# Kernel tuning notes

Hardware: AMD Instinct MI355X
Metric: run time of the kernel (lower is better)

Reference implementation:

```python
import jax, jax.numpy as jnp
import numpy as np

NEG_SLOPE = 0.2
N_NODES = 51200      # batch 256 graphs x 200 nodes
NODE_PER_G = 200
IN_DIM = 200
HID = 64
HEADS = 4
N_CLASSES = 2
E_RAND = 16 * N_NODES


def setup_inputs() -> dict:
    key = jax.random.key(0)
    ks = jax.random.split(key, 12)
    feat = jax.random.normal(ks[0], (N_NODES, IN_DIM), dtype=jnp.float32)
    # random edges kept within each 200-node graph block + self-loops (no zero in-degree)
    g_off = (jnp.arange(E_RAND) % (N_NODES // NODE_PER_G)) * NODE_PER_G
    src = jax.random.randint(ks[1], (E_RAND,), 0, NODE_PER_G) + g_off
    dst = jax.random.randint(ks[2], (E_RAND,), 0, NODE_PER_G) + g_off
    loop = jnp.arange(N_NODES)
    src = jnp.concatenate([src, loop]).astype(jnp.int32)
    dst = jnp.concatenate([dst, loop]).astype(jnp.int32)
    s = 0.05
    W0 = jax.random.normal(ks[3], (IN_DIM, HEADS * HID), dtype=jnp.float32) * s
    al0 = jax.random.normal(ks[4], (HEADS, HID), dtype=jnp.float32) * s
    ar0 = jax.random.normal(ks[5], (HEADS, HID), dtype=jnp.float32) * s
    W1 = jax.random.normal(ks[6], (HEADS * HID, HEADS * HID), dtype=jnp.float32) * s
    al1 = jax.random.normal(ks[7], (HEADS, HID), dtype=jnp.float32) * s
    ar1 = jax.random.normal(ks[8], (HEADS, HID), dtype=jnp.float32) * s
    Wc = jax.random.normal(ks[9], (NODE_PER_G * HID, N_CLASSES), dtype=jnp.float32) * s
    bc = jnp.zeros((N_CLASSES,), dtype=jnp.float32)
    return {"feat": feat, "src": src, "dst": dst, "W0": W0, "al0": al0, "ar0": ar0,
            "W1": W1, "al1": al1, "ar1": ar1, "Wc": Wc, "bc": bc, "batch_size": 256}


def gat_conv(h, src, dst, W, al, ar, residual):
    N = h.shape[0]
    ft = (h @ W).reshape(N, HEADS, HID)                      # [N,H,D]
    el = jnp.einsum('nhd,hd->nh', ft, al)                    # [N,H]
    er = jnp.einsum('nhd,hd->nh', ft, ar)
    e = jax.nn.leaky_relu(el[src] + er[dst], NEG_SLOPE)      # [E,H]
    emax = jax.ops.segment_max(e, dst, num_segments=N)
    a = jnp.exp(e - emax[dst])
    denom = jax.ops.segment_sum(a, dst, num_segments=N)
    alpha = a / denom[dst]                                   # [E,H]
    out = jax.ops.segment_sum(alpha[:, :, None] * ft[src], dst, num_segments=N)
    if residual:
        out = out + h.reshape(N, HEADS, HID)                 # identity residual (in==H*D)
    return jax.nn.elu(out)                                   # [N,H,D]


def reference(feat, src, dst, W0, al0, ar0, W1, al1, ar1, Wc, bc, batch_size):
    h = gat_conv(feat, src, dst, W0, al0, ar0, residual=False)
    h = h.reshape(h.shape[0], HEADS * HID)                   # flatten(1)
    h = gat_conv(h, src, dst, W1, al1, ar1, residual=True)
    h = h.mean(axis=1)                                       # mean over heads -> [N,D]
    h = h.reshape(batch_size, -1)                            # [B, node*D]
    return h @ Wc + bc
```

## Files before the change

### kernel.cpp

```cpp
#include <hip/hip_runtime.h>
#include <hip/hip_bf16.h>
#include <hip/hip_fp16.h>

#define N_NODES_C   51200
#define NODE_PER_G  200
#define NGRAPH      256
#define HEADS       4
#define HID         64
#define FDIM        256
#define IN_DIM_C    200
#define E_RAND_C    819200
#define RAND_PER_G  3200
#define AWS         3208
#define NEG_SLOPE   0.2f

typedef _Float16 f16x8 __attribute__((ext_vector_type(8)));
typedef float    f32x4 __attribute__((ext_vector_type(4)));

__device__ __forceinline__ float leaky(float x) { return fmaxf(x, NEG_SLOPE * x); }

__global__ __launch_bounds__(256) void transpose_both(
    const float* __restrict__ W0, const float* __restrict__ W1,
    _Float16* __restrict__ W0t, _Float16* __restrict__ W1t)
{
    int k = blockIdx.x, n = threadIdx.x;
    if (k < IN_DIM_C)
        W0t[(size_t)n * IN_DIM_C + k] = (_Float16)W0[(size_t)k * FDIM + n];
    else {
        int kk = k - IN_DIM_C;
        W1t[(size_t)n * FDIM + kk] = (_Float16)W1[(size_t)kk * FDIM + n];
    }
}

__global__ __launch_bounds__(1024) void build_csr(
    const int* __restrict__ src, const int* __restrict__ dst,
    uchar2* __restrict__ egs, int* __restrict__ goff)
{
    __shared__ uchar2 s_e[RAND_PER_G];
    __shared__ int s_cnt[256];
    __shared__ int s_off[256];

    const int g = blockIdx.x, tid = threadIdx.x;
    const int node0 = g * NODE_PER_G;
    uchar2* egsp = egs + (size_t)g * RAND_PER_G;

    if (tid < 256) s_cnt[tid] = 0;
    __syncthreads();
    for (int e = tid; e < RAND_PER_G; e += 1024) {
        int eid = g + (e << 8);
        uchar2 ed = make_uchar2((unsigned char)(src[eid] - node0),
                                (unsigned char)(dst[eid] - node0));
        s_e[e] = ed;
        atomicAdd(&s_cnt[ed.y], 1);
    }
    __syncthreads();
    if (tid < 64) {
        const int base = tid << 2;
        int c0_ = s_cnt[base], c1 = s_cnt[base + 1];
        int c2 = s_cnt[base + 2], c3 = s_cnt[base + 3];
        s_cnt[base] = 0; s_cnt[base + 1] = 0;
        s_cnt[base + 2] = 0; s_cnt[base + 3] = 0;
        int s1 = c0_ + c1, s2 = s1 + c2, s3 = s2 + c3;
        int pre = s3;
#pragma unroll
        for (int d = 1; d < 64; d <<= 1) {
            int t = __shfl_up(pre, d);
            if (tid >= d) pre += t;
        }
        int excl = pre - s3;
        s_off[base]     = excl;
        s_off[base + 1] = excl + c0_;
        s_off[base + 2] = excl + s1;
        s_off[base + 3] = excl + s2;
    }
    __syncthreads();
    for (int e = tid; e < RAND_PER_G; e += 1024) {
        uchar2 ed = s_e[e];
        int pos = s_off[ed.y] + atomicAdd(&s_cnt[ed.y], 1);
        egsp[pos] = ed;
    }
    if (tid <= NODE_PER_G)
        goff[(size_t)g * 201 + tid] = s_off[tid];
}

__device__ __forceinline__ int swzoff(int m, int kg) {
    int pair = m >> 1;
    int slot = (((m & 1) << 2) | kg) ^ (pair & 7);
    return pair * 64 + slot * 8;
}

__device__ __forceinline__ f16x8 cvt8(float4 a, float4 b) {
    f16x8 r;
    r[0] = (_Float16)a.x; r[1] = (_Float16)a.y;
    r[2] = (_Float16)a.z; r[3] = (_Float16)a.w;
    r[4] = (_Float16)b.x; r[5] = (_Float16)b.y;
    r[6] = (_Float16)b.z; r[7] = (_Float16)b.w;
    return r;
}

template <bool L1>
__global__ __launch_bounds__(1024) void fused_gat(
    const void* __restrict__ A_, const _Float16* __restrict__ Bt, int K,
    const uchar2* __restrict__ egs, const int* __restrict__ goff,
    const float* __restrict__ al, const float* __restrict__ ar,
    const _Float16* __restrict__ hprev, const float* __restrict__ Wc,
    const float* __restrict__ bc, void* __restrict__ out_)
{
    __shared__ __align__(16) _Float16 s_ft[NODE_PER_G * FDIM];
    __shared__ __align__(16) unsigned s_aw[HEADS * AWS];
    __shared__ float s_el[NODE_PER_G * HEADS];
    __shared__ float s_er[NODE_PER_G * HEADS];
    __shared__ int   s_off[NODE_PER_G + 1];
    __shared__ float s_red[2];

    const int g = blockIdx.x, tid = threadIdx.x;
    const int node0 = g * NODE_PER_G;
    const int wave = tid >> 6, lane = tid & 63;
    const uchar2* egp = egs + (size_t)g * RAND_PER_G;

    if (tid < 2) s_red[tid] = 0.f;
    if (tid <= NODE_PER_G) s_off[tid] = goff[(size_t)g * 201 + tid];

    {
        _Float16* sA = (_Float16*)s_aw;
        _Float16* sB = (_Float16*)s_aw + 208 * 32;
        const int arow = tid >> 2;
        const int agk  = tid & 3;
        const int KC = (K + 31) >> 5;
        const int aoffL = swzoff(lane & 15, lane >> 4);
        const uint4 z4 = make_uint4(0u, 0u, 0u, 0u);

        f32x4 acc[4][4];
#pragma unroll
        for (int t = 0; t < 4; ++t)
#pragma unroll
            for (int ni = 0; ni < 4; ++ni) acc[t][ni] = (f32x4){0.f, 0.f, 0.f, 0.f};

        for (int kc = 0; kc < KC; ++kc) {
            const int k8 = kc * 32 + agk * 8;
            __syncthreads();
            if (arow < 208) {
                if constexpr (L1) {
                    const _Float16* A = (const _Float16*)A_;
                    uint4 v = (arow < NODE_PER_G && k8 + 8 <= K)
                        ? *(const uint4*)&A[(size_t)(node0 + arow) * K + k8] : z4;
                    *(uint4*)&sA[swzoff(arow, agk)] = v;
                } else {
                    const float* A = (const float*)A_;
                    float4 x = make_float4(0.f, 0.f, 0.f, 0.f), y = x;
                    if (arow < NODE_PER_G && k8 + 8 <= K) {
                        const float* pa = &A[(size_t)(node0 + arow) * K + k8];
                        x = *(const float4*)pa;
                        y = *(const float4*)(pa + 4);
                    }
                    *(f16x8*)&sA[swzoff(arow, agk)] = cvt8(x, y);
                }
            }
            {
                uint4 v = (k8 + 8 <= K)
                    ? *(const uint4*)&Bt[(size_t)arow * K + k8] : z4;
                *(uint4*)&sB[swzoff(arow, agk)] = v;
            }
            __syncthreads();
#pragma unroll
            for (int t = 0; t < 4; ++t) {
                const int task = wave * 4 + t;
                if (task < 52) {
                    const int m16 = task >> 2, n64 = task & 3;
                    f16x8 af = *(const f16x8*)&sA[aoffL + m16 * 512];
#pragma unroll
                    for (int ni = 0; ni < 4; ++ni) {
                        f16x8 bf = *(const f16x8*)&sB[aoffL + n64 * 2048 + ni * 512];
                        acc[t][ni] = __builtin_amdgcn_mfma_f32_16x16x32_f16(
                            af, bf, acc[t][ni], 0, 0, 0);
                    }
                }
            }
        }
        __syncthreads();
#pragma unroll
        for (int t = 0; t < 4; ++t) {
            const int task = wave * 4 + t;
            if (task < 52) {
                const int m16 = task >> 2, n64 = task & 3;
                const int r0 = m16 * 16 + ((lane >> 4) << 2);
                const int cc = n64 * 64 + (lane & 15);
#pragma unroll
                for (int ni = 0; ni < 4; ++ni)
#pragma unroll
                    for (int r = 0; r < 4; ++r) {
                        int row = r0 + r;
                        if (row < NODE_PER_G)
                            s_ft[row * FDIM + cc + ni * 16] =
                                (_Float16)acc[t][ni][r];
                    }
            }
        }
    }
    __syncthreads();

    {
        const int lh = lane >> 4, ld = (lane & 15) * 4;
        float4 alv = *(const float4*)&al[lh * HID + ld];
        float4 arv = *(const float4*)&ar[lh * HID + ld];
        for (int n = wave; n < NODE_PER_G; n += 16) {
            uint2 gr = *(const uint2*)&s_ft[n * FDIM + lane * 4];
            float2 f01 = __half22float2(*(__half2*)&gr.x);
            float2 f23 = __half22float2(*(__half2*)&gr.y);
            float pl = f01.x * alv.x + f01.y * alv.y + f23.x * alv.z + f23.y * alv.w;
            float pr = f01.x * arv.x + f01.y * arv.y + f23.x * arv.z + f23.y * arv.w;
#pragma unroll
            for (int m = 1; m < 16; m <<= 1) {
                pl += __shfl_xor(pl, m);
                pr += __shfl_xor(pr, m);
            }
            if ((lane & 15) == 0) {
                s_el[n * 4 + lh] = pl;
                s_er[n * 4 + lh] = pr;
            }
        }
    }
    __syncthreads();

    for (int e = tid; e < RAND_PER_G; e += 1024) {
        uchar2 ed = egp[e];
        float4 elv = *(const float4*)&s_el[ed.x * 4];
        float4 erv = *(const float4*)&s_er[ed.y * 4];
        unsigned sb = (unsigned)ed.x << 16;
        __half h0 = __float2half_rn(__expf(leaky(elv.x + erv.x)));
        __half h1 = __float2half_rn(__expf(leaky(elv.y + erv.y)));
        __half h2 = __float2half_rn(__expf(leaky(elv.z + erv.z)));
        __half h3 = __float2half_rn(__expf(leaky(elv.w + erv.w)));
        s_aw[e]           = sb | (unsigned)__half_as_ushort(h0);
        s_aw[AWS + e]     = sb | (unsigned)__half_as_ushort(h1);
        s_aw[2 * AWS + e] = sb | (unsigned)__half_as_ushort(h2);
        s_aw[3 * AWS + e] = sb | (unsigned)__half_as_ushort(h3);
    }
    __syncthreads();

    const int half = lane >> 5;
    const int l32 = lane & 31;
    const int c0 = l32 * 8;
    const int hh = l32 >> 3;
    const unsigned* awp = s_aw + hh * AWS;
    const __half hz = __ushort_as_half((unsigned short)0);
    float w0 = 0.f, w1 = 0.f;

    for (int p = wave; p < NODE_PER_G / 2; p += 16) {
        const int n = half ? (p + 100) : p;
        const int begA = s_off[p],       lenA = s_off[p + 1] - begA;
        const int begB = s_off[p + 100], lenB = s_off[p + 101] - begB;
        const int beg = half ? begB : begA;
        const int len = half ? lenB : lenA;
        const int jmax = max(lenA, lenB);

        float a_self = __expf(leaky(s_el[n * 4 + hh] + s_er[n * 4 + hh]));
        __half asumh = __float2half_rn(a_self);
        __half2 as2 = __half2half2(asumh);
        __half2 acc2[4], acc2b[4];
        {
            uint4 v = *(const uint4*)&s_ft[n * FDIM + c0];
            const __half2* hv = (const __half2*)&v;
#pragma unroll
            for (int q = 0; q < 4; ++q) {
                acc2[q]  = __hmul2(as2, hv[q]);
                acc2b[q] = __half2half2(hz);
            }
        }

        int j = 0;
        for (; j + 2 <= jmax; j += 2) {
            unsigned wd0 = awp[(j < len)     ? (beg + j)     : 0];
            unsigned wd1 = awp[(j + 1 < len) ? (beg + j + 1) : 0];
            __half a0 = (j < len)     ? __ushort_as_half((unsigned short)wd0) : hz;
            __half a1 = (j + 1 < len) ? __ushort_as_half((unsigned short)wd1) : hz;
            uint4 v0 = *(const uint4*)&s_ft[(int)(wd0 >> 16) * FDIM + c0];
            uint4 v1 = *(const uint4*)&s_ft[(int)(wd1 >> 16) * FDIM + c0];
            asumh = __hadd(asumh, __hadd(a0, a1));
            __half2 a02 = __half2half2(a0), a12 = __half2half2(a1);
            const __half2* h0v = (const __half2*)&v0;
            const __half2* h1v = (const __half2*)&v1;
#pragma unroll
            for (int q = 0; q < 4; ++q) {
                acc2[q]  = __hfma2(a02, h0v[q], acc2[q]);
                acc2b[q] = __hfma2(a12, h1v[q], acc2b[q]);
            }
        }
        if (j < jmax) {
            unsigned wd0 = awp[(j < len) ? (beg + j) : 0];
            __half a0 = (j < len) ? __ushort_as_half((unsigned short)wd0) : hz;
            uint4 v0 = *(const uint4*)&s_ft[(int)(wd0 >> 16) * FDIM + c0];
            asumh = __hadd(asumh, a0);
            __half2 a02 = __half2half2(a0);
            const __half2* h0v = (const __half2*)&v0;
#pragma unroll
            for (int q = 0; q < 4; ++q)
                acc2[q] = __hfma2(a02, h0v[q], acc2[q]);
        }

        float acc[8];
#pragma unroll
        for (int q = 0; q < 4; ++q) {
            float2 f = __half22float2(__hadd2(acc2[q], acc2b[q]));
            acc[2 * q] = f.x;
            acc[2 * q + 1] = f.y;
        }
        const float rd = 1.f / __half2float(asumh);
#pragma unroll
        for (int q = 0; q < 8; ++q) acc[q] *= rd;

        if constexpr (L1) {
            uint4 rv = *(const uint4*)&hprev[(size_t)(node0 + n) * FDIM + c0];
            const __half2* hv = (const __half2*)&rv;
#pragma unroll
            for (int q = 0; q < 4; ++q) {
                float2 f = __half22float2(hv[q]);
                acc[2 * q]     += f.x;
                acc[2 * q + 1] += f.y;
            }
#pragma unroll
            for (int q = 0; q < 8; ++q)
                acc[q] = (acc[q] > 0.f) ? acc[q] : expm1f(acc[q]);
#pragma unroll
            for (int q = 0; q < 8; ++q) {
                acc[q] += __shfl_xor(acc[q], 8);
                acc[q] += __shfl_xor(acc[q], 16);
            }
            if (l32 < 8) {
                const int d0 = l32 * 8;
                const float* wp = &Wc[((size_t)n * HID + d0) * 2];
#pragma unroll
                for (int q = 0; q < 8; ++q) {
                    float m = acc[q] * 0.25f;
                    w0 += m * wp[2 * q];
                    w1 += m * wp[2 * q + 1];
                }
            }
        } else {
#pragma unroll
            for (int q = 0; q < 8; ++q)
                acc[q] = (acc[q] > 0.f) ? acc[q] : expm1f(acc[q]);
            __half2 o[4];
#pragma unroll
            for (int q = 0; q < 4; ++q) {
                o[q].x = __float2half_rn(acc[2 * q]);
                o[q].y = __float2half_rn(acc[2 * q + 1]);
            }
            _Float16* outp = (_Float16*)out_;
            *(uint4*)&outp[(size_t)(node0 + n) * FDIM + c0] = *(uint4*)o;
        }
    }

    if constexpr (L1) {
#pragma unroll
        for (int m = 32; m >= 1; m >>= 1) {
            w0 += __shfl_xor(w0, m);
            w1 += __shfl_xor(w1, m);
        }
        if (lane == 0) {
            atomicAdd(&s_red[0], w0);
            atomicAdd(&s_red[1], w1);
        }
        __syncthreads();
        if (tid < 2) ((float*)out_)[g * 2 + tid] = s_red[tid] + bc[tid];
    }
}

extern "C" void kernel_launch(void* const* d_in, const int* in_sizes, int n_in,
                              void* d_out, int out_size, void* d_ws, size_t ws_size,
                              hipStream_t stream) {
    const float* feat = (const float*)d_in[0];
    const int*   src  = (const int*)d_in[1];
    const int*   dst  = (const int*)d_in[2];
    const float* W0   = (const float*)d_in[3];
    const float* al0  = (const float*)d_in[4];
    const float* ar0  = (const float*)d_in[5];
    const float* W1   = (const float*)d_in[6];
    const float* al1  = (const float*)d_in[7];
    const float* ar1  = (const float*)d_in[8];
    const float* Wc   = (const float*)d_in[9];
    const float* bc   = (const float*)d_in[10];
    float* out = (float*)d_out;

    _Float16* h0  = (_Float16*)d_ws;
    _Float16* W0t = h0 + (size_t)N_NODES_C * FDIM;
    _Float16* W1t = W0t + (size_t)FDIM * IN_DIM_C;
    uchar2*   egs = (uchar2*)(W1t + (size_t)FDIM * FDIM);
    int*      goff = (int*)(egs + (size_t)NGRAPH * RAND_PER_G);

    build_csr<<<NGRAPH, 1024, 0, stream>>>(src, dst, egs, goff);
    transpose_both<<<IN_DIM_C + FDIM, 256, 0, stream>>>(W0, W1, W0t, W1t);

    fused_gat<false><<<NGRAPH, 1024, 0, stream>>>(
        feat, W0t, IN_DIM_C, egs, goff, al0, ar0, nullptr, nullptr, nullptr, h0);

    fused_gat<true><<<NGRAPH, 1024, 0, stream>>>(
        h0, W1t, FDIM, egs, goff, al1, ar1, h0, Wc, bc, out);
}
```

Baseline: 121.7 us.

## Split each graph across two blocks by head pair to double grid parallelism

```diff
diff --git a/kernel.cpp b/kernel.cpp
--- a/kernel.cpp
+++ b/kernel.cpp
@@ -11,7 +11,7 @@
 #define IN_DIM_C    200
 #define E_RAND_C    819200
 #define RAND_PER_G  3200
-#define AWS         3208
+#define AWS         3204
 #define NEG_SLOPE   0.2f
 
 typedef _Float16 f16x8 __attribute__((ext_vector_type(8)));
@@ -106,14 +106,15 @@
     const _Float16* __restrict__ hprev, const float* __restrict__ Wc,
     const float* __restrict__ bc, void* __restrict__ out_)
 {
-    __shared__ __align__(16) _Float16 s_ft[NODE_PER_G * FDIM];
-    __shared__ __align__(16) unsigned s_aw[HEADS * AWS];
-    __shared__ float s_el[NODE_PER_G * HEADS];
-    __shared__ float s_er[NODE_PER_G * HEADS];
+    __shared__ __align__(16) _Float16 s_ft[NODE_PER_G * 128];
+    __shared__ __align__(16) unsigned s_aw[2 * AWS];
+    __shared__ float s_el[NODE_PER_G * 2];
+    __shared__ float s_er[NODE_PER_G * 2];
     __shared__ int   s_off[NODE_PER_G + 1];
     __shared__ float s_red[2];
 
-    const int g = blockIdx.x, tid = threadIdx.x;
+    const int g = blockIdx.x >> 1, hp = blockIdx.x & 1;
+    const int tid = threadIdx.x;
     const int node0 = g * NODE_PER_G;
     const int wave = tid >> 6, lane = tid & 63;
     const uchar2* egp = egs + (size_t)g * RAND_PER_G;
@@ -130,9 +131,9 @@
         const int aoffL = swzoff(lane & 15, lane >> 4);
         const uint4 z4 = make_uint4(0u, 0u, 0u, 0u);
 
-        f32x4 acc[4][4];
-#pragma unroll
-        for (int t = 0; t < 4; ++t)
+        f32x4 acc[2][4];
+#pragma unroll
+        for (int t = 0; t < 2; ++t)
 #pragma unroll
             for (int ni = 0; ni < 4; ++ni) acc[t][ni] = (f32x4){0.f, 0.f, 0.f, 0.f};
 
@@ -156,17 +157,17 @@
                     *(f16x8*)&sA[swzoff(arow, agk)] = cvt8(x, y);
                 }
             }
-            {
+            if (arow < 128) {
                 uint4 v = (k8 + 8 <= K)
-                    ? *(const uint4*)&Bt[(size_t)arow * K + k8] : z4;
+                    ? *(const uint4*)&Bt[(size_t)(hp * 128 + arow) * K + k8] : z4;
                 *(uint4*)&sB[swzoff(arow, agk)] = v;
             }
             __syncthreads();
 #pragma unroll
-            for (int t = 0; t < 4; ++t) {
-                const int task = wave * 4 + t;
-                if (task < 52) {
-                    const int m16 = task >> 2, n64 = task & 3;
+            for (int t = 0; t < 2; ++t) {
+                const int task = wave * 2 + t;
+                if (task < 26) {
+                    const int m16 = task >> 1, n64 = task & 1;
                     f16x8 af = *(const f16x8*)&sA[aoffL + m16 * 512];
 #pragma unroll
                     for (int ni = 0; ni < 4; ++ni) {
@@ -179,10 +180,10 @@
         }
         __syncthreads();
 #pragma unroll
-        for (int t = 0; t < 4; ++t) {
-            const int task = wave * 4 + t;
-            if (task < 52) {
-                const int m16 = task >> 2, n64 = task & 3;
+        for (int t = 0; t < 2; ++t) {
+            const int task = wave * 2 + t;
+            if (task < 26) {
+                const int m16 = task >> 1, n64 = task & 1;
                 const int r0 = m16 * 16 + ((lane >> 4) << 2);
                 const int cc = n64 * 64 + (lane & 15);
 #pragma unroll
@@ -191,7 +192,7 @@
                     for (int r = 0; r < 4; ++r) {
                         int row = r0 + r;
                         if (row < NODE_PER_G)
-                            s_ft[row * FDIM + cc + ni * 16] =
+                            s_ft[row * 128 + cc + ni * 16] =
                                 (_Float16)acc[t][ni][r];
                     }
             }
@@ -200,23 +201,25 @@
     __syncthreads();
 
     {
-        const int lh = lane >> 4, ld = (lane & 15) * 4;
-        float4 alv = *(const float4*)&al[lh * HID + ld];
-        float4 arv = *(const float4*)&ar[lh * HID + ld];
+        const int lh = lane >> 5;
+        const int ld = (lane & 31) * 2;
+        const float* alh = al + (hp * 2 + lh) * HID + ld;
+        const float* arh = ar + (hp * 2 + lh) * HID + ld;
+        float2 alv = make_float2(alh[0], alh[1]);
+        float2 arv = make_float2(arh[0], arh[1]);
         for (int n = wave; n < NODE_PER_G; n += 16) {
-            uint2 gr = *(const uint2*)&s_ft[n * FDIM + lane * 4];
-            float2 f01 = __half22float2(*(__half2*)&gr.x);
-            float2 f23 = __half22float2(*(__half2*)&gr.y);
-            float pl = f01.x * alv.x + f01.y * alv.y + f23.x * alv.z + f23.y * alv.w;
-            float pr = f01.x * arv.x + f01.y * arv.y + f23.x * arv.z + f23.y * arv.w;
-#pragma unroll
-            for (int m = 1; m < 16; m <<= 1) {
+            unsigned gr = *(const unsigned*)&s_ft[n * 128 + lh * 64 + ld];
+            float2 f = __half22float2(*(__half2*)&gr);
+            float pl = f.x * alv.x + f.y * alv.y;
+            float pr = f.x * arv.x + f.y * arv.y;
+#pragma unroll
+            for (int m = 1; m < 32; m <<= 1) {
                 pl += __shfl_xor(pl, m);
                 pr += __shfl_xor(pr, m);
             }
-            if ((lane & 15) == 0) {
-                s_el[n * 4 + lh] = pl;
-                s_er[n * 4 + lh] = pr;
+            if ((lane & 31) == 0) {
+                s_el[n * 2 + lh] = pl;
+                s_er[n * 2 + lh] = pr;
             }
         }
     }
@@ -224,24 +227,20 @@
 
     for (int e = tid; e < RAND_PER_G; e += 1024) {
         uchar2 ed = egp[e];
-        float4 elv = *(const float4*)&s_el[ed.x * 4];
-        float4 erv = *(const float4*)&s_er[ed.y * 4];
+        float2 elv = *(const float2*)&s_el[ed.x * 2];
+        float2 erv = *(const float2*)&s_er[ed.y * 2];
         unsigned sb = (unsigned)ed.x << 16;
-        __half h0 = __float2half_rn(__expf(leaky(elv.x + erv.x)));
-        __half h1 = __float2half_rn(__expf(leaky(elv.y + erv.y)));
-        __half h2 = __float2half_rn(__expf(leaky(elv.z + erv.z)));
-        __half h3 = __float2half_rn(__expf(leaky(elv.w + erv.w)));
-        s_aw[e]           = sb | (unsigned)__half_as_ushort(h0);
-        s_aw[AWS + e]     = sb | (unsigned)__half_as_ushort(h1);
-        s_aw[2 * AWS + e] = sb | (unsigned)__half_as_ushort(h2);
-        s_aw[3 * AWS + e] = sb | (unsigned)__half_as_ushort(h3);
+        __half ha = __float2half_rn(__expf(leaky(elv.x + erv.x)));
+        __half hb = __float2half_rn(__expf(leaky(elv.y + erv.y)));
+        s_aw[e]       = sb | (unsigned)__half_as_ushort(ha);
+        s_aw[AWS + e] = sb | (unsigned)__half_as_ushort(hb);
     }
     __syncthreads();
 
     const int half = lane >> 5;
     const int l32 = lane & 31;
-    const int c0 = l32 * 8;
-    const int hh = l32 >> 3;
+    const int c0 = l32 * 4;
+    const int hh = l32 >> 4;
     const unsigned* awp = s_aw + hh * AWS;
     const __half hz = __ushort_as_half((unsigned short)0);
     float w0 = 0.f, w1 = 0.f;
@@ -254,18 +253,17 @@
         const int len = half ? lenB : lenA;
         const int jmax = max(lenA, lenB);
 
-        float a_self = __expf(leaky(s_el[n * 4 + hh] + s_er[n * 4 + hh]));
+        float a_self = __expf(leaky(s_el[n * 2 + hh] + s_er[n * 2 + hh]));
         __half asumh = __float2half_rn(a_self);
         __half2 as2 = __half2half2(asumh);
-        __half2 acc2[4], acc2b[4];
+        __half2 acc2[2], acc2b[2];
         {
-            uint4 v = *(const uint4*)&s_ft[n * FDIM + c0];
+            uint2 v = *(const uint2*)&s_ft[n * 128 + c0];
             const __half2* hv = (const __half2*)&v;
-#pragma unroll
-            for (int q = 0; q < 4; ++q) {
-                acc2[q]  = __hmul2(as2, hv[q]);
-                acc2b[q] = __half2half2(hz);
-            }
+            acc2[0] = __hmul2(as2, hv[0]);
+            acc2[1] = __hmul2(as2, hv[1]);
+            acc2b[0] = __half2half2(hz);
+            acc2b[1] = __half2half2(hz);
         }
 
         int j = 0;
@@ -274,63 +272,55 @@
             unsigned wd1 = awp[(j + 1 < len) ? (beg + j + 1) : 0];
             __half a0 = (j < len)     ? __ushort_as_half((unsigned short)wd0) : hz;
             __half a1 = (j + 1 < len) ? __ushort_as_half((unsigned short)wd1) : hz;
-            uint4 v0 = *(const uint4*)&s_ft[(int)(wd0 >> 16) * FDIM + c0];
-            uint4 v1 = *(const uint4*)&s_ft[(int)(wd1 >> 16) * FDIM + c0];
+            uint2 v0 = *(const uint2*)&s_ft[(int)(wd0 >> 16) * 128 + c0];
+            uint2 v1 = *(const uint2*)&s_ft[(int)(wd1 >> 16) * 128 + c0];
             asumh = __hadd(asumh, __hadd(a0, a1));
             __half2 a02 = __half2half2(a0), a12 = __half2half2(a1);
             const __half2* h0v = (const __half2*)&v0;
             const __half2* h1v = (const __half2*)&v1;
-#pragma unroll
-            for (int q = 0; q < 4; ++q) {
-                acc2[q]  = __hfma2(a02, h0v[q], acc2[q]);
-                acc2b[q] = __hfma2(a12, h1v[q], acc2b[q]);
-            }
+            acc2[0]  = __hfma2(a02, h0v[0], acc2[0]);
+            acc2[1]  = __hfma2(a02, h0v[1], acc2[1]);
+            acc2b[0] = __hfma2(a12, h1v[0], acc2b[0]);
+            acc2b[1] = __hfma2(a12, h1v[1], acc2b[1]);
         }
         if (j < jmax) {
             unsigned wd0 = awp[(j < len) ? (beg + j) : 0];
             __half a0 = (j < len) ? __ushort_as_half((unsigned short)wd0) : hz;
-            uint4 v0 = *(const uint4*)&s_ft[(int)(wd0 >> 16) * FDIM + c0];
+            uint2 v0 = *(const uint2*)&s_ft[(int)(wd0 >> 16) * 128 + c0];
             asumh = __hadd(asumh, a0);
             __half2 a02 = __half2half2(a0);
             const __half2* h0v = (const __half2*)&v0;
+            acc2[0] = __hfma2(a02, h0v[0], acc2[0]);
+            acc2[1] = __hfma2(a02, h0v[1], acc2[1]);
+        }
+
+        float acc[4];
+        {
+            float2 f0 = __half22float2(__hadd2(acc2[0], acc2b[0]));
+            float2 f1 = __half22float2(__hadd2(acc2[1], acc2b[1]));
+            acc[0] = f0.x; acc[1] = f0.y; acc[2] = f1.x; acc[3] = f1.y;
+        }
+        const float rd = 1.f / __half2float(asumh);
+#pragma unroll
+        for (int q = 0; q < 4; ++q) acc[q] *= rd;
+
+        if constexpr (L1) {
+            uint2 rv = *(const uint2*)&hprev[(size_t)(node0 + n) * FDIM + hp * 128 + c0];
+            const __half2* hv = (const __half2*)&rv;
+            float2 r0 = __half22float2(hv[0]);
+            float2 r1 = __half22float2(hv[1]);
+            acc[0] += r0.x; acc[1] += r0.y; acc[2] += r1.x; acc[3] += r1.y;
 #pragma unroll
             for (int q = 0; q < 4; ++q)
-                acc2[q] = __hfma2(a02, h0v[q], acc2[q]);
-        }
-
-        float acc[8];
-#pragma unroll
-        for (int q = 0; q < 4; ++q) {
-            float2 f = __half22float2(__hadd2(acc2[q], acc2b[q]));
-            acc[2 * q] = f.x;
-            acc[2 * q + 1] = f.y;
-        }
-        const float rd = 1.f / __half2float(asumh);
-#pragma unroll
-        for (int q = 0; q < 8; ++q) acc[q] *= rd;
-
-        if constexpr (L1) {
-            uint4 rv = *(const uint4*)&hprev[(size_t)(node0 + n) * FDIM + c0];
-            const __half2* hv = (const __half2*)&rv;
-#pragma unroll
-            for (int q = 0; q < 4; ++q) {
-                float2 f = __half22float2(hv[q]);
-                acc[2 * q]     += f.x;
-                acc[2 * q + 1] += f.y;
-            }
-#pragma unroll
-            for (int q = 0; q < 8; ++q)
                 acc[q] = (acc[q] > 0.f) ? acc[q] : expm1f(acc[q]);
 #pragma unroll
-            for (int q = 0; q < 8; ++q) {
-                acc[q] += __shfl_xor(acc[q], 8);
+            for (int q = 0; q < 4; ++q)
                 acc[q] += __shfl_xor(acc[q], 16);
-            }
-            if (l32 < 8) {
-                const int d0 = l32 * 8;
+            if (l32 < 16) {
+                const int d0 = l32 * 4;
                 const float* wp = &Wc[((size_t)n * HID + d0) * 2];
 #pragma unroll
-                for (int q = 0; q < 8; ++q) {
+                for (int q = 0; q < 4; ++q) {
                     float m = acc[q] * 0.25f;
                     w0 += m * wp[2 * q];
                     w1 += m * wp[2 * q + 1];
@@ -338,16 +328,13 @@
             }
         } else {
 #pragma unroll
-            for (int q = 0; q < 8; ++q)
+            for (int q = 0; q < 4; ++q)
                 acc[q] = (acc[q] > 0.f) ? acc[q] : expm1f(acc[q]);
-            __half2 o[4];
-#pragma unroll
-            for (int q = 0; q < 4; ++q) {
-                o[q].x = __float2half_rn(acc[2 * q]);
-                o[q].y = __float2half_rn(acc[2 * q + 1]);
-            }
+            __half2 o[2];
+            o[0].x = __float2half_rn(acc[0]); o[0].y = __float2half_rn(acc[1]);
+            o[1].x = __float2half_rn(acc[2]); o[1].y = __float2half_rn(acc[3]);
             _Float16* outp = (_Float16*)out_;
-            *(uint4*)&outp[(size_t)(node0 + n) * FDIM + c0] = *(uint4*)o;
+            *(uint2*)&outp[(size_t)(node0 + n) * FDIM + hp * 128 + c0] = *(uint2*)o;
         }
     }
 
@@ -362,7 +349,13 @@
             atomicAdd(&s_red[1], w1);
         }
         __syncthreads();
-        if (tid < 2) ((float*)out_)[g * 2 + tid] = s_red[tid] + bc[tid];
+        if (tid == 0) {
+            float* out = (float*)out_;
+            float b0 = hp ? 0.f : bc[0];
+            float b1 = hp ? 0.f : bc[1];
+            atomicAdd(&out[g * 2 + 0], s_red[0] + b0);
+            atomicAdd(&out[g * 2 + 1], s_red[1] + b1);
+        }
     }
 }
 
@@ -390,10 +383,11 @@
 
     build_csr<<<NGRAPH, 1024, 0, stream>>>(src, dst, egs, goff);
     transpose_both<<<IN_DIM_C + FDIM, 256, 0, stream>>>(W0, W1, W0t, W1t);
-
-    fused_gat<false><<<NGRAPH, 1024, 0, stream>>>(
+    hipMemsetAsync(d_out, 0, (size_t)NGRAPH * 2 * sizeof(float), stream);
+
+    fused_gat<false><<<NGRAPH * 2, 1024, 0, stream>>>(
         feat, W0t, IN_DIM_C, egs, goff, al0, ar0, nullptr, nullptr, nullptr, h0);
 
-    fused_gat<true><<<NGRAPH, 1024, 0, stream>>>(
+    fused_gat<true><<<NGRAPH * 2, 1024, 0, stream>>>(
         h0, W1t, FDIM, egs, goff, al1, ar1, h0, Wc, bc, out);
 }
```

New measurement: 141.4 us. 1.16x slower.

## Recast edge aggregation as dense per-graph attention matmul on MFMA

Applied to the files above, without the earlier changes.

```diff
diff --git a/kernel.cpp b/kernel.cpp
--- a/kernel.cpp
+++ b/kernel.cpp
@@ -11,7 +11,8 @@
 #define IN_DIM_C    200
 #define E_RAND_C    819200
 #define RAND_PER_G  3200
-#define AWS         3208
+#define EPG         3400
+#define SRCP        208
 #define NEG_SLOPE   0.2f
 
 typedef _Float16 f16x8 __attribute__((ext_vector_type(8)));
@@ -19,39 +20,46 @@
 
 __device__ __forceinline__ float leaky(float x) { return fmaxf(x, NEG_SLOPE * x); }
 
-__global__ __launch_bounds__(256) void transpose_both(
+__global__ __launch_bounds__(1024) void build_csr(
+    const int* __restrict__ src, const int* __restrict__ dst,
+    uchar4* __restrict__ egs, int* __restrict__ goff,
     const float* __restrict__ W0, const float* __restrict__ W1,
     _Float16* __restrict__ W0t, _Float16* __restrict__ W1t)
 {
-    int k = blockIdx.x, n = threadIdx.x;
-    if (k < IN_DIM_C)
-        W0t[(size_t)n * IN_DIM_C + k] = (_Float16)W0[(size_t)k * FDIM + n];
-    else {
-        int kk = k - IN_DIM_C;
-        W1t[(size_t)n * FDIM + kk] = (_Float16)W1[(size_t)kk * FDIM + n];
-    }
-}
-
-__global__ __launch_bounds__(1024) void build_csr(
-    const int* __restrict__ src, const int* __restrict__ dst,
-    uchar2* __restrict__ egs, int* __restrict__ goff)
-{
-    __shared__ uchar2 s_e[RAND_PER_G];
+    __shared__ uchar2 s_u[EPG];
+    __shared__ uchar2 s_s[EPG];
     __shared__ int s_cnt[256];
     __shared__ int s_off[256];
 
     const int g = blockIdx.x, tid = threadIdx.x;
     const int node0 = g * NODE_PER_G;
-    uchar2* egsp = egs + (size_t)g * RAND_PER_G;
+
+    {
+        int idx = g * 1024 + tid;
+        if (idx < (IN_DIM_C + FDIM) * FDIM) {
+            int k = idx >> 8, n = idx & 255;
+            if (k < IN_DIM_C)
+                W0t[(size_t)n * IN_DIM_C + k] = (_Float16)W0[(size_t)k * FDIM + n];
+            else {
+                int kk = k - IN_DIM_C;
+                W1t[(size_t)n * FDIM + kk] = (_Float16)W1[(size_t)kk * FDIM + n];
+            }
+        }
+    }
 
     if (tid < 256) s_cnt[tid] = 0;
     __syncthreads();
-    for (int e = tid; e < RAND_PER_G; e += 1024) {
-        int eid = g + (e << 8);
-        uchar2 ed = make_uchar2((unsigned char)(src[eid] - node0),
-                                (unsigned char)(dst[eid] - node0));
-        s_e[e] = ed;
-        atomicAdd(&s_cnt[ed.y], 1);
+    for (int e = tid; e < EPG; e += 1024) {
+        int sl, dl;
+        if (e < RAND_PER_G) {
+            int eid = g + (e << 8);
+            sl = src[eid] - node0;
+            dl = dst[eid] - node0;
+        } else {
+            sl = dl = e - RAND_PER_G;
+        }
+        s_u[e] = make_uchar2((unsigned char)sl, (unsigned char)dl);
+        atomicAdd(&s_cnt[dl], 1);
     }
     __syncthreads();
     if (tid < 64) {
@@ -74,10 +82,30 @@
         s_off[base + 3] = excl + s2;
     }
     __syncthreads();
-    for (int e = tid; e < RAND_PER_G; e += 1024) {
-        uchar2 ed = s_e[e];
+    for (int e = tid; e < EPG; e += 1024) {
+        uchar2 ed = s_u[e];
         int pos = s_off[ed.y] + atomicAdd(&s_cnt[ed.y], 1);
-        egsp[pos] = ed;
+        s_s[pos] = ed;
+    }
+    __syncthreads();
+    if (tid < NODE_PER_G) {
+        const int beg = s_off[tid], end = s_off[tid + 1];
+        uchar4* outp = egs + (size_t)g * EPG;
+        int w = beg;
+        for (int i = beg; i < end; ++i) {
+            int s0 = s_s[i].x;
+            bool first = true;
+            for (int j = beg; j < i; ++j)
+                if (s_s[j].x == s0) { first = false; break; }
+            if (first) {
+                int c = 1;
+                for (int j = i + 1; j < end; ++j)
+                    if (s_s[j].x == s0) ++c;
+                outp[w++] = make_uchar4((unsigned char)s0, (unsigned char)tid,
+                                        (unsigned char)c, 0);
+            }
+        }
+        while (w < end) outp[w++] = make_uchar4(0, 0, 0, 0);
     }
     if (tid <= NODE_PER_G)
         goff[(size_t)g * 201 + tid] = s_off[tid];
@@ -101,29 +129,30 @@
 template <bool L1>
 __global__ __launch_bounds__(1024) void fused_gat(
     const void* __restrict__ A_, const _Float16* __restrict__ Bt, int K,
-    const uchar2* __restrict__ egs, const int* __restrict__ goff,
+    const uchar4* __restrict__ egs, const int* __restrict__ goff,
     const float* __restrict__ al, const float* __restrict__ ar,
     const _Float16* __restrict__ hprev, const float* __restrict__ Wc,
     const float* __restrict__ bc, void* __restrict__ out_)
 {
-    __shared__ __align__(16) _Float16 s_ft[NODE_PER_G * FDIM];
-    __shared__ __align__(16) unsigned s_aw[HEADS * AWS];
+    __shared__ __align__(16) _Float16 s_ftT[256 * SRCP];
+    __shared__ __align__(16) _Float16 s_p[112 * SRCP];
     __shared__ float s_el[NODE_PER_G * HEADS];
     __shared__ float s_er[NODE_PER_G * HEADS];
-    __shared__ int   s_off[NODE_PER_G + 1];
+    __shared__ float s_den[NODE_PER_G * HEADS];
+    __shared__ unsigned short s_off16[NODE_PER_G + 1];
     __shared__ float s_red[2];
 
     const int g = blockIdx.x, tid = threadIdx.x;
     const int node0 = g * NODE_PER_G;
     const int wave = tid >> 6, lane = tid & 63;
-    const uchar2* egp = egs + (size_t)g * RAND_PER_G;
+    const uchar4* egp = egs + (size_t)g * EPG;
 
     if (tid < 2) s_red[tid] = 0.f;
-    if (tid <= NODE_PER_G) s_off[tid] = goff[(size_t)g * 201 + tid];
+    if (tid <= NODE_PER_G) s_off16[tid] = (unsigned short)goff[(size_t)g * 201 + tid];
 
     {
-        _Float16* sA = (_Float16*)s_aw;
-        _Float16* sB = (_Float16*)s_aw + 208 * 32;
+        _Float16* sA = s_p;
+        _Float16* sB = s_p + 208 * 32;
         const int arow = tid >> 2;
         const int agk  = tid & 3;
         const int KC = (K + 31) >> 5;
@@ -178,177 +207,133 @@
             }
         }
         __syncthreads();
+        const int c = lane & 15;
 #pragma unroll
         for (int t = 0; t < 4; ++t) {
             const int task = wave * 4 + t;
             if (task < 52) {
                 const int m16 = task >> 2, n64 = task & 3;
                 const int r0 = m16 * 16 + ((lane >> 4) << 2);
-                const int cc = n64 * 64 + (lane & 15);
-#pragma unroll
-                for (int ni = 0; ni < 4; ++ni)
-#pragma unroll
-                    for (int r = 0; r < 4; ++r) {
-                        int row = r0 + r;
-                        if (row < NODE_PER_G)
-                            s_ft[row * FDIM + cc + ni * 16] =
-                                (_Float16)acc[t][ni][r];
-                    }
-            }
-        }
-    }
-    __syncthreads();
-
-    {
-        const int lh = lane >> 4, ld = (lane & 15) * 4;
-        float4 alv = *(const float4*)&al[lh * HID + ld];
-        float4 arv = *(const float4*)&ar[lh * HID + ld];
-        for (int n = wave; n < NODE_PER_G; n += 16) {
-            uint2 gr = *(const uint2*)&s_ft[n * FDIM + lane * 4];
-            float2 f01 = __half22float2(*(__half2*)&gr.x);
-            float2 f23 = __half22float2(*(__half2*)&gr.y);
-            float pl = f01.x * alv.x + f01.y * alv.y + f23.x * alv.z + f23.y * alv.w;
-            float pr = f01.x * arv.x + f01.y * arv.y + f23.x * arv.z + f23.y * arv.w;
-#pragma unroll
-            for (int m = 1; m < 16; m <<= 1) {
-                pl += __shfl_xor(pl, m);
-                pr += __shfl_xor(pr, m);
-            }
-            if ((lane & 15) == 0) {
-                s_el[n * 4 + lh] = pl;
-                s_er[n * 4 + lh] = pr;
-            }
-        }
-    }
-    __syncthreads();
-
-    for (int e = tid; e < RAND_PER_G; e += 1024) {
-        uchar2 ed = egp[e];
-        float4 elv = *(const float4*)&s_el[ed.x * 4];
-        float4 erv = *(const float4*)&s_er[ed.y * 4];
-        unsigned sb = (unsigned)ed.x << 16;
-        __half h0 = __float2half_rn(__expf(leaky(elv.x + erv.x)));
-        __half h1 = __float2half_rn(__expf(leaky(elv.y + erv.y)));
-        __half h2 = __float2half_rn(__expf(leaky(elv.z + erv.z)));
-        __half h3 = __float2half_rn(__expf(leaky(elv.w + erv.w)));
-        s_aw[e]           = sb | (unsigned)__half_as_ushort(h0);
-        s_aw[AWS + e]     = sb | (unsigned)__half_as_ushort(h1);
-        s_aw[2 * AWS + e] = sb | (unsigned)__half_as_ushort(h2);
-        s_aw[3 * AWS + e] = sb | (unsigned)__half_as_ushort(h3);
-    }
-    __syncthreads();
-
-    const int half = lane >> 5;
-    const int l32 = lane & 31;
-    const int c0 = l32 * 8;
-    const int hh = l32 >> 3;
-    const unsigned* awp = s_aw + hh * AWS;
-    const __half hz = __ushort_as_half((unsigned short)0);
+                float alv[4], arv[4];
+#pragma unroll
+                for (int ni = 0; ni < 4; ++ni) {
+                    alv[ni] = al[n64 * 64 + ni * 16 + c];
+                    arv[ni] = ar[n64 * 64 + ni * 16 + c];
+                }
+#pragma unroll
+                for (int r = 0; r < 4; ++r) {
+                    const int node = r0 + r;
+                    float e_l = 0.f, e_r = 0.f;
+#pragma unroll
+                    for (int ni = 0; ni < 4; ++ni) {
+                        float v = acc[t][ni][r];
+                        e_l = fmaf(v, alv[ni], e_l);
+                        e_r = fmaf(v, arv[ni], e_r);
+                        s_ftT[(n64 * 64 + ni * 16 + c) * SRCP + node] =
+                            (_Float16)v;
+                    }
+#pragma unroll
+                    for (int m = 1; m < 16; m <<= 1) {
+                        e_l += __shfl_xor(e_l, m);
+                        e_r += __shfl_xor(e_r, m);
+                    }
+                    if (c == 0 && node < NODE_PER_G) {
+                        s_el[node * 4 + n64] = e_l;
+                        s_er[node * 4 + n64] = e_r;
+                    }
+                }
+            }
+        }
+    }
+    __syncthreads();
+
+    if (tid < NODE_PER_G * HEADS) {
+        const int d = tid >> 2, h = tid & 3;
+        const int beg = s_off16[d], end = s_off16[d + 1];
+        const float ern = s_er[d * 4 + h];
+        float den = 0.f;
+        for (int i = beg; i < end; ++i) {
+            uchar4 E = egp[i];
+            if (!E.z) break;
+            den += (float)E.z * __expf(leaky(s_el[(int)E.x * 4 + h] + ern));
+        }
+        s_den[tid] = den;
+    }
+    __syncthreads();
+
     float w0 = 0.f, w1 = 0.f;
-
-    for (int p = wave; p < NODE_PER_G / 2; p += 16) {
-        const int n = half ? (p + 100) : p;
-        const int begA = s_off[p],       lenA = s_off[p + 1] - begA;
-        const int begB = s_off[p + 100], lenB = s_off[p + 101] - begB;
-        const int beg = half ? begB : begA;
-        const int len = half ? lenB : lenA;
-        const int jmax = max(lenA, lenB);
-
-        float a_self = __expf(leaky(s_el[n * 4 + hh] + s_er[n * 4 + hh]));
-        __half asumh = __float2half_rn(a_self);
-        __half2 as2 = __half2half2(asumh);
-        __half2 acc2[4], acc2b[4];
-        {
-            uint4 v = *(const uint4*)&s_ft[n * FDIM + c0];
-            const __half2* hv = (const __half2*)&v;
-#pragma unroll
-            for (int q = 0; q < 4; ++q) {
-                acc2[q]  = __hmul2(as2, hv[q]);
-                acc2b[q] = __half2half2(hz);
-            }
-        }
-
-        int j = 0;
-        for (; j + 2 <= jmax; j += 2) {
-            unsigned wd0 = awp[(j < len)     ? (beg + j)     : 0];
-            unsigned wd1 = awp[(j + 1 < len) ? (beg + j + 1) : 0];
-            __half a0 = (j < len)     ? __ushort_as_half((unsigned short)wd0) : hz;
-            __half a1 = (j + 1 < len) ? __ushort_as_half((unsigned short)wd1) : hz;
-            uint4 v0 = *(const uint4*)&s_ft[(int)(wd0 >> 16) * FDIM + c0];
-            uint4 v1 = *(const uint4*)&s_ft[(int)(wd1 >> 16) * FDIM + c0];
-            asumh = __hadd(asumh, __hadd(a0, a1));
-            __half2 a02 = __half2half2(a0), a12 = __half2half2(a1);
-            const __half2* h0v = (const __half2*)&v0;
-            const __half2* h1v = (const __half2*)&v1;
-#pragma unroll
-            for (int q = 0; q < 4; ++q) {
-                acc2[q]  = __hfma2(a02, h0v[q], acc2[q]);
-                acc2b[q] = __hfma2(a12, h1v[q], acc2b[q]);
-            }
-        }
-        if (j < jmax) {
-            unsigned wd0 = awp[(j < len) ? (beg + j) : 0];
-            __half a0 = (j < len) ? __ushort_as_half((unsigned short)wd0) : hz;
-            uint4 v0 = *(const uint4*)&s_ft[(int)(wd0 >> 16) * FDIM + c0];
-            asumh = __hadd(asumh, a0);
-            __half2 a02 = __half2half2(a0);
-            const __half2* h0v = (const __half2*)&v0;
-#pragma unroll
-            for (int q = 0; q < 4; ++q)
-                acc2[q] = __hfma2(a02, h0v[q], acc2[q]);
-        }
-
-        float acc[8];
-#pragma unroll
-        for (int q = 0; q < 4; ++q) {
-            float2 f = __half22float2(__hadd2(acc2[q], acc2b[q]));
-            acc[2 * q] = f.x;
-            acc[2 * q + 1] = f.y;
-        }
-        const float rd = 1.f / __half2float(asumh);
-#pragma unroll
-        for (int q = 0; q < 8; ++q) acc[q] *= rd;
-
-        if constexpr (L1) {
-            uint4 rv = *(const uint4*)&hprev[(size_t)(node0 + n) * FDIM + c0];
-            const __half2* hv = (const __half2*)&rv;
-#pragma unroll
-            for (int q = 0; q < 4; ++q) {
-                float2 f = __half22float2(hv[q]);
-                acc[2 * q]     += f.x;
-                acc[2 * q + 1] += f.y;
-            }
-#pragma unroll
-            for (int q = 0; q < 8; ++q)
-                acc[q] = (acc[q] > 0.f) ? acc[q] : expm1f(acc[q]);
-#pragma unroll
-            for (int q = 0; q < 8; ++q) {
-                acc[q] += __shfl_xor(acc[q], 8);
-                acc[q] += __shfl_xor(acc[q], 16);
-            }
-            if (l32 < 8) {
-                const int d0 = l32 * 8;
-                const float* wp = &Wc[((size_t)n * HID + d0) * 2];
-#pragma unroll
-                for (int q = 0; q < 8; ++q) {
-                    float m = acc[q] * 0.25f;
-                    w0 += m * wp[2 * q];
-                    w1 += m * wp[2 * q + 1];
-                }
-            }
-        } else {
-#pragma unroll
-            for (int q = 0; q < 8; ++q)
-                acc[q] = (acc[q] > 0.f) ? acc[q] : expm1f(acc[q]);
-            __half2 o[4];
-#pragma unroll
-            for (int q = 0; q < 4; ++q) {
-                o[q].x = __float2half_rn(acc[2 * q]);
-                o[q].y = __float2half_rn(acc[2 * q + 1]);
-            }
-            _Float16* outp = (_Float16*)out_;
-            *(uint4*)&outp[(size_t)(node0 + n) * FDIM + c0] = *(uint4*)o;
-        }
+    for (int pass = 0; pass < 8; ++pass) {
+        const int h = pass >> 1, tile = pass & 1;
+        const int t0 = tile * 112;
+        for (int i = tid; i < 112 * SRCP / 8; i += 1024)
+            *(uint4*)&s_p[i * 8] = make_uint4(0u, 0u, 0u, 0u);
+        __syncthreads();
+        for (int e = tid; e < EPG; e += 1024) {
+            uchar4 E = egp[e];
+            int dl = (int)E.y - t0;
+            if (E.z && (unsigned)dl < 112u) {
+                float s = s_el[(int)E.x * 4 + h] + s_er[(int)E.y * 4 + h];
+                s_p[dl * SRCP + (int)E.x] =
+                    (_Float16)((float)E.z * __expf(leaky(s)));
+            }
+        }
+        __syncthreads();
+        if (wave < 14) {
+            const int m16 = wave >> 1, nh = wave & 1;
+            const int rowA  = m16 * 16 + (lane & 15);
+            const int rowB0 = h * 64 + nh * 32 + (lane & 15);
+            const int rowB1 = rowB0 + 16;
+            const int kg = (lane >> 4) << 3;
+            f32x4 c0 = {0.f, 0.f, 0.f, 0.f}, c1 = {0.f, 0.f, 0.f, 0.f};
+#pragma unroll
+            for (int ks = 0; ks < 6; ++ks) {
+                const int k0 = ks * 32 + kg;
+                f16x8 af = *(const f16x8*)&s_p[rowA * SRCP + k0];
+                f16x8 b0 = *(const f16x8*)&s_ftT[rowB0 * SRCP + k0];
+                f16x8 b1 = *(const f16x8*)&s_ftT[rowB1 * SRCP + k0];
+                c0 = __builtin_amdgcn_mfma_f32_16x16x32_f16(af, b0, c0, 0, 0, 0);
+                c1 = __builtin_amdgcn_mfma_f32_16x16x32_f16(af, b1, c1, 0, 0, 0);
+            }
+            {
+                const bool hi = (kg >= 16);
+                const int kb = hi ? 0 : (192 + kg);
+                f16x8 af = *(const f16x8*)&s_p[rowA * SRCP + kb];
+                f16x8 b0 = *(const f16x8*)&s_ftT[rowB0 * SRCP + kb];
+                f16x8 b1 = *(const f16x8*)&s_ftT[rowB1 * SRCP + kb];
+                if (hi) {
+#pragma unroll
+                    for (int i = 0; i < 8; ++i) af[i] = (_Float16)0.f;
+                }
+                c0 = __builtin_amdgcn_mfma_f32_16x16x32_f16(af, b0, c0, 0, 0, 0);
+                c1 = __builtin_amdgcn_mfma_f32_16x16x32_f16(af, b1, c1, 0, 0, 0);
+            }
+#pragma unroll
+            for (int r = 0; r < 4; ++r) {
+                const int d = t0 + m16 * 16 + ((lane >> 4) << 2) + r;
+                if (d < NODE_PER_G) {
+                    const float rd = 1.f / s_den[d * 4 + h];
+                    float v0 = c0[r] * rd, v1 = c1[r] * rd;
+                    if constexpr (L1) {
+                        v0 += (float)hprev[(size_t)(node0 + d) * FDIM + rowB0];
+                        v1 += (float)hprev[(size_t)(node0 + d) * FDIM + rowB1];
+                    }
+                    v0 = (v0 > 0.f) ? v0 : expm1f(v0);
+                    v1 = (v1 > 0.f) ? v1 : expm1f(v1);
+                    if constexpr (L1) {
+                        const int d0 = rowB0 & 63, d1 = rowB1 & 63;
+                        float2 wa = ((const float2*)Wc)[d * HID + d0];
+                        float2 wb = ((const float2*)Wc)[d * HID + d1];
+                        w0 += 0.25f * (v0 * wa.x + v1 * wb.x);
+                        w1 += 0.25f * (v0 * wa.y + v1 * wb.y);
+                    } else {
+                        _Float16* outp = (_Float16*)out_;
+                        outp[(size_t)(node0 + d) * FDIM + rowB0] = (_Float16)v0;
+                        outp[(size_t)(node0 + d) * FDIM + rowB1] = (_Float16)v1;
+                    }
+                }
+            }
+        }
+        __syncthreads();
     }
 
     if constexpr (L1) {
@@ -385,11 +370,10 @@
     _Float16* h0  = (_Float16*)d_ws;
     _Float16* W0t = h0 + (size_t)N_NODES_C * FDIM;
     _Float16* W1t = W0t + (size_t)FDIM * IN_DIM_C;
-    uchar2*   egs = (uchar2*)(W1t + (size_t)FDIM * FDIM);
-    int*      goff = (int*)(egs + (size_t)NGRAPH * RAND_PER_G);
-
-    build_csr<<<NGRAPH, 1024, 0, stream>>>(src, dst, egs, goff);
-    transpose_both<<<IN_DIM_C + FDIM, 256, 0, stream>>>(W0, W1, W0t, W1t);
+    uchar4*   egs = (uchar4*)(W1t + (size_t)FDIM * FDIM);
+    int*      goff = (int*)(egs + (size_t)NGRAPH * EPG);
+
+    build_csr<<<NGRAPH, 1024, 0, stream>>>(src, dst, egs, goff, W0, W1, W0t, W1t);
 
     fused_gat<false><<<NGRAPH, 1024, 0, stream>>>(
         feat, W0t, IN_DIM_C, egs, goff, al0, ar0, nullptr, nullptr, nullptr, h0);
```

New measurement: 221.0 us. 1.82x slower.
